# Kernel optimization log

Measured on AMD Instinct MI355X. Metric: run time of the kernel, lower is better.

Reference implementation:

```python
import jax, jax.numpy as jnp
import numpy as np

NQ = 4          # wires=4 in the PennyLane device
NLAYERS = 4     # num_layers default
AX = 'abcd'     # one einsum letter per qubit axis


def _apply_1q(state, U, w):
    """Apply a 2x2 (or batched (B,2,2)) unitary to qubit axis w of state (B,2,2,2,2)."""
    sub = AX[w]
    out = AX[:w] + 'x' + AX[w + 1:]
    if U.ndim == 3:
        return jnp.einsum(f'zx{sub},z{AX}->z{out}', U, state)
    return jnp.einsum(f'x{sub},z{AX}->z{out}', U, state)


def _apply_cnot(state, c, t):
    """CNOT with control qubit c, target qubit t (static wire indices)."""
    s0 = jax.lax.index_in_dim(state, 0, axis=c + 1, keepdims=True)
    s1 = jax.lax.index_in_dim(state, 1, axis=c + 1, keepdims=True)
    s1 = jnp.flip(s1, axis=t + 1)  # flip target amplitudes where control = 1
    return jnp.concatenate([s0, s1], axis=c + 1)


def _rot(phi, theta, omega):
    """PennyLane Rot gate: RZ(omega) @ RY(theta) @ RZ(phi), as a 2x2 complex matrix."""
    c = jnp.cos(theta * 0.5)
    s = jnp.sin(theta * 0.5)
    em = jnp.exp(-0.5j * (phi + omega))   # e^{-i(phi+omega)/2}, complex64 (weak 1j)
    ed = jnp.exp(0.5j * (phi - omega))    # e^{+i(phi-omega)/2}
    return jnp.stack([
        jnp.stack([em * c, -ed * s]),
        jnp.stack([jnp.conj(ed) * s, jnp.conj(em) * c]),
    ])


def _forward(inputs, q_weights):
    B = inputs.shape[0]
    # |0000> statevector, batched
    state = jnp.zeros((B, 2 ** NQ), jnp.complex64).at[:, 0].set(1.0)
    state = state.reshape((B,) + (2,) * NQ)

    # AngleEmbedding with rotation='Y': RY(x_w) on each wire w (per-sample angles)
    half = inputs * 0.5
    c, s = jnp.cos(half), jnp.sin(half)
    for w in range(NQ):
        U = jnp.stack([jnp.stack([c[:, w], -s[:, w]], axis=-1),
                       jnp.stack([s[:, w], c[:, w]], axis=-1)], axis=-2)
        state = _apply_1q(state, U.astype(jnp.complex64), w)

    # One StronglyEntanglingLayers block per layer of q_weights:
    # per-qubit Rot gates followed by a ring of CNOTs (range r=1 for single-layer calls)
    n_layers = q_weights.shape[0]
    for l in range(n_layers):
        for w in range(NQ):
            state = _apply_1q(state, _rot(q_weights[l, w, 0],
                                          q_weights[l, w, 1],
                                          q_weights[l, w, 2]), w)
        for w in range(NQ):
            state = _apply_cnot(state, w, (w + 1) % NQ)

    # <Z_i> for each wire: marginal prob of bit i, contracted with diag(+1,-1)
    probs = state.real ** 2 + state.imag ** 2  # (B,2,2,2,2)
    z = jnp.array([1.0, -1.0], jnp.float32)
    expvals = []
    for w in range(NQ):
        reduce_axes = tuple(i + 1 for i in range(NQ) if i != w)
        p = probs.sum(axis=reduce_axes)  # (B,2)
        expvals.append(p @ z)
    return jnp.stack(expvals, axis=-1)  # (B,4)


def setup_inputs() -> dict:
    key = jax.random.key(0)
    k1, k2 = jax.random.split(key)
    B = 1048576
    inputs = jax.random.normal(k1, (B, NQ), dtype=jnp.float32)
    # glorot_uniform for shape (4,4,3): limit = sqrt(6/(fan_in+fan_out))
    limit = np.sqrt(6.0 / (NQ * 3 + NQ * 3)).astype(np.float32)
    q_weights = jax.random.uniform(k2, (NLAYERS, NQ, 3), dtype=jnp.float32,
                                   minval=-limit, maxval=limit)
    return {"inputs": inputs, "q_weights": q_weights}


def reference(inputs, q_weights):
    return _forward(inputs, q_weights)
```

## Files before the change

kernel.cpp:

```cpp
#include <hip/hip_runtime.h>
#include <math.h>


__global__ void build_unitary(const float* __restrict__ qw, float* __restrict__ U) {
    __shared__ float g[16][8];
    int t = threadIdx.x;
    if (t < 16) {
        float phi = qw[t * 3 + 0], theta = qw[t * 3 + 1], omega = qw[t * 3 + 2];
        float ct = cosf(0.5f * theta), st = sinf(0.5f * theta);
        float ha = 0.5f * (phi + omega), hd = 0.5f * (phi - omega);
        float emr = cosf(ha), emi = -sinf(ha);
        float edr = cosf(hd), edi =  sinf(hd);
        g[t][0] =  emr * ct; g[t][1] =  emi * ct;
        g[t][2] = -edr * st; g[t][3] = -edi * st;
        g[t][4] =  edr * st; g[t][5] = -edi * st;
        g[t][6] =  emr * ct; g[t][7] = -emi * ct;
    }
    __syncthreads();
    if (t >= 16) return;
    float ar[16], ai[16];
#pragma unroll
    for (int b = 0; b < 16; ++b) { ar[b] = (b == t) ? 1.f : 0.f; ai[b] = 0.f; }
#pragma unroll
    for (int l = 0; l < 4; ++l) {
#pragma unroll
        for (int w = 0; w < 4; ++w) {
            int gi = l * 4 + w;
            float u00r = g[gi][0], u00i = g[gi][1], u01r = g[gi][2], u01i = g[gi][3];
            float u10r = g[gi][4], u10i = g[gi][5], u11r = g[gi][6], u11i = g[gi][7];
            int mask = 8 >> w;
#pragma unroll
            for (int b = 0; b < 16; ++b) {
                if (b & mask) continue;
                int b1 = b | mask;
                float xr = ar[b], xi = ai[b], yr = ar[b1], yi = ai[b1];
                ar[b]  = u00r * xr - u00i * xi + u01r * yr - u01i * yi;
                ai[b]  = u00r * xi + u00i * xr + u01r * yi + u01i * yr;
                ar[b1] = u10r * xr - u10i * xi + u11r * yr - u11i * yi;
                ai[b1] = u10r * xi + u10i * xr + u11r * yi + u11i * yr;
            }
        }
#pragma unroll
        for (int w = 0; w < 4; ++w) {
            int cm = 8 >> w, tm = 8 >> ((w + 1) & 3);
#pragma unroll
            for (int b = 0; b < 16; ++b) {
                if ((b & cm) && !(b & tm)) {
                    int b1 = b | tm;
                    float tr = ar[b], ti = ai[b];
                    ar[b] = ar[b1]; ai[b] = ai[b1];
                    ar[b1] = tr;    ai[b1] = ti;
                }
            }
        }
    }
#pragma unroll
    for (int b = 0; b < 16; ++b) {
        U[t * 32 + b]      = ar[b];
        U[t * 32 + 16 + b] = ai[b];
    }
}

__global__ __launch_bounds__(256) void qlayer_main(
        const float4* __restrict__ x, const float* __restrict__ U,
        float4* __restrict__ out, int B) {
    __shared__ float svs[256 * 17];
    int tid = threadIdx.x;
    int i = blockIdx.x * 256 + tid;
    if (i >= B) return;

    float4 xv = x[i];
    float c0, s0, c1, s1, c2, s2, c3, s3;
    __sincosf(0.5f * xv.x, &s0, &c0);
    __sincosf(0.5f * xv.y, &s1, &c1);
    __sincosf(0.5f * xv.z, &s2, &c2);
    __sincosf(0.5f * xv.w, &s3, &c3);
    float p01[4] = {c0 * c1, c0 * s1, s0 * c1, s0 * s1};
    float p23[4] = {c2 * c3, c2 * s3, s2 * c3, s2 * s3};
    float* mysv = &svs[tid * 17];
#pragma unroll
    for (int a = 0; a < 4; ++a)
#pragma unroll
        for (int b = 0; b < 4; ++b) mysv[a * 4 + b] = p01[a] * p23[b];

    float are[16], aim[16];
#pragma unroll
    for (int b = 0; b < 16; ++b) { are[b] = 0.f; aim[b] = 0.f; }
#pragma unroll 2
    for (int j = 0; j < 16; ++j) {
        float sj = mysv[j];
        const float* row = U + j * 32;
#pragma unroll
        for (int b = 0; b < 16; ++b) {
            are[b] = fmaf(row[b],      sj, are[b]);
            aim[b] = fmaf(row[16 + b], sj, aim[b]);
        }
    }

    float p[16];
#pragma unroll
    for (int b = 0; b < 16; ++b) p[b] = fmaf(are[b], are[b], aim[b] * aim[b]);

    float s8[8], d8[8];
#pragma unroll
    for (int k = 0; k < 8; ++k) { s8[k] = p[2*k] + p[2*k+1]; d8[k] = p[2*k] - p[2*k+1]; }
    float e3 = ((d8[0]+d8[1])+(d8[2]+d8[3]))+((d8[4]+d8[5])+(d8[6]+d8[7]));
    float u4[4], v4[4];
#pragma unroll
    for (int m = 0; m < 4; ++m) { u4[m] = s8[2*m] + s8[2*m+1]; v4[m] = s8[2*m] - s8[2*m+1]; }
    float e2 = (v4[0]+v4[1])+(v4[2]+v4[3]);
    float x0 = u4[0]+u4[1], x1 = u4[2]+u4[3];
    float y0 = u4[0]-u4[1], y1 = u4[2]-u4[3];
    float e1 = y0 + y1;
    float e0 = x0 - x1;

    out[i] = make_float4(e0, e1, e2, e3);
}

extern "C" void kernel_launch(void* const* d_in, const int* in_sizes, int n_in,
                              void* d_out, int out_size, void* d_ws, size_t ws_size,
                              hipStream_t stream) {
    const float4* x  = (const float4*)d_in[0];
    const float*  qw = (const float*)d_in[1];
    float* U = (float*)d_ws;
    float4* out = (float4*)d_out;
    int B = in_sizes[0] / 4;

    hipLaunchKernelGGL(build_unitary, dim3(1), dim3(64), 0, stream, qw, U);

    int blocks = (B + 255) / 256;
    hipLaunchKernelGGL(qlayer_main, dim3(blocks), dim3(256), 0, stream,
                       x, U, out, B);
}
```

Measured before the change: 92.75 us.

## Precompute Pauli-basis coefficient tensor so each sample evaluates a trigonometric polynomial

```diff
diff --git a/kernel.cpp b/kernel.cpp
--- a/kernel.cpp
+++ b/kernel.cpp
@@ -2,9 +2,13 @@
 #include <math.h>
 
 
-__global__ void build_unitary(const float* __restrict__ qw, float* __restrict__ U) {
+__global__ void build_C(const float* __restrict__ qw, float* __restrict__ Cg) {
     __shared__ float g[16][8];
+    __shared__ float Ur[16][16];
+    __shared__ float Ui[16][16];
+    __shared__ float ReE[4][16][16];
     int t = threadIdx.x;
+
     if (t < 16) {
         float phi = qw[t * 3 + 0], theta = qw[t * 3 + 1], omega = qw[t * 3 + 2];
         float ct = cosf(0.5f * theta), st = sinf(0.5f * theta);
@@ -17,103 +21,126 @@
         g[t][6] =  emr * ct; g[t][7] = -emi * ct;
     }
     __syncthreads();
-    if (t >= 16) return;
-    float ar[16], ai[16];
+
+    if (t < 16) {
+        float ar[16], ai[16];
 #pragma unroll
-    for (int b = 0; b < 16; ++b) { ar[b] = (b == t) ? 1.f : 0.f; ai[b] = 0.f; }
+        for (int b = 0; b < 16; ++b) { ar[b] = (b == t) ? 1.f : 0.f; ai[b] = 0.f; }
 #pragma unroll
-    for (int l = 0; l < 4; ++l) {
+        for (int l = 0; l < 4; ++l) {
 #pragma unroll
-        for (int w = 0; w < 4; ++w) {
-            int gi = l * 4 + w;
-            float u00r = g[gi][0], u00i = g[gi][1], u01r = g[gi][2], u01i = g[gi][3];
-            float u10r = g[gi][4], u10i = g[gi][5], u11r = g[gi][6], u11i = g[gi][7];
-            int mask = 8 >> w;
+            for (int w = 0; w < 4; ++w) {
+                int gi = l * 4 + w;
+                float u00r = g[gi][0], u00i = g[gi][1], u01r = g[gi][2], u01i = g[gi][3];
+                float u10r = g[gi][4], u10i = g[gi][5], u11r = g[gi][6], u11i = g[gi][7];
+                int mask = 8 >> w;
 #pragma unroll
-            for (int b = 0; b < 16; ++b) {
-                if (b & mask) continue;
-                int b1 = b | mask;
-                float xr = ar[b], xi = ai[b], yr = ar[b1], yi = ai[b1];
-                ar[b]  = u00r * xr - u00i * xi + u01r * yr - u01i * yi;
-                ai[b]  = u00r * xi + u00i * xr + u01r * yi + u01i * yr;
-                ar[b1] = u10r * xr - u10i * xi + u11r * yr - u11i * yi;
-                ai[b1] = u10r * xi + u10i * xr + u11r * yi + u11i * yr;
+                for (int b = 0; b < 16; ++b) {
+                    if (b & mask) continue;
+                    int b1 = b | mask;
+                    float xr = ar[b], xi = ai[b], yr = ar[b1], yi = ai[b1];
+                    ar[b]  = u00r * xr - u00i * xi + u01r * yr - u01i * yi;
+                    ai[b]  = u00r * xi + u00i * xr + u01r * yi + u01i * yr;
+                    ar[b1] = u10r * xr - u10i * xi + u11r * yr - u11i * yi;
+                    ai[b1] = u10r * xi + u10i * xr + u11r * yi + u11i * yr;
+                }
+            }
+#pragma unroll
+            for (int w = 0; w < 4; ++w) {
+                int cm = 8 >> w, tm = 8 >> ((w + 1) & 3);
+#pragma unroll
+                for (int b = 0; b < 16; ++b) {
+                    if ((b & cm) && !(b & tm)) {
+                        int b1 = b | tm;
+                        float tr = ar[b], ti = ai[b];
+                        ar[b] = ar[b1]; ai[b] = ai[b1];
+                        ar[b1] = tr;    ai[b1] = ti;
+                    }
+                }
             }
         }
 #pragma unroll
-        for (int w = 0; w < 4; ++w) {
-            int cm = 8 >> w, tm = 8 >> ((w + 1) & 3);
+        for (int b = 0; b < 16; ++b) { Ur[b][t] = ar[b]; Ui[b][t] = ai[b]; }
+    }
+    __syncthreads();
+
+    for (int idx = t; idx < 1024; idx += 256) {
+        int w = idx >> 8, i = (idx >> 4) & 15, j = idx & 15;
+        float acc = 0.f;
 #pragma unroll
-            for (int b = 0; b < 16; ++b) {
-                if ((b & cm) && !(b & tm)) {
-                    int b1 = b | tm;
-                    float tr = ar[b], ti = ai[b];
-                    ar[b] = ar[b1]; ai[b] = ai[b1];
-                    ar[b1] = tr;    ai[b1] = ti;
-                }
-            }
+        for (int b = 0; b < 16; ++b) {
+            float z = ((b >> (3 - w)) & 1) ? -1.f : 1.f;
+            acc += z * (Ur[b][i] * Ur[b][j] + Ui[b][i] * Ui[b][j]);
         }
+        ReE[w][i][j] = acc;
     }
+    __syncthreads();
+
+    for (int idx = t; idx < 324; idx += 256) {
+        int w = idx & 3, tt = idx >> 2;
+        int t01 = tt / 9, t23 = tt % 9;
+        int tq[4] = { t01 / 3, t01 % 3, t23 / 3, t23 % 3 };
+        int xmask = 0, zmask = 0;
 #pragma unroll
-    for (int b = 0; b < 16; ++b) {
-        U[t * 32 + b]      = ar[b];
-        U[t * 32 + 16 + b] = ai[b];
+        for (int k = 0; k < 4; ++k) {
+            if (tq[k] == 1) xmask |= 8 >> k;
+            if (tq[k] == 2) zmask |= 8 >> k;
+        }
+        float acc = 0.f;
+#pragma unroll
+        for (int i = 0; i < 16; ++i) {
+            float sgn = (__popc(i & zmask) & 1) ? -1.f : 1.f;
+            acc += sgn * ReE[w][i][i ^ xmask];
+        }
+        Cg[idx] = acc * 0.0625f;
     }
 }
 
 __global__ __launch_bounds__(256) void qlayer_main(
-        const float4* __restrict__ x, const float* __restrict__ U,
+        const float4* __restrict__ x, const float* __restrict__ Cg,
         float4* __restrict__ out, int B) {
-    __shared__ float svs[256 * 17];
-    int tid = threadIdx.x;
-    int i = blockIdx.x * 256 + tid;
+    __shared__ __align__(16) float C[324];
+    for (int k = threadIdx.x; k < 324; k += 256) C[k] = Cg[k];
+    __syncthreads();
+
+    int i = blockIdx.x * 256 + threadIdx.x;
     if (i >= B) return;
+    float4 xv = x[i];
+    float s0, c0, s1, c1, s2, c2, s3, c3;
+    __sincosf(xv.x, &s0, &c0);
+    __sincosf(xv.y, &s1, &c1);
+    __sincosf(xv.z, &s2, &c2);
+    __sincosf(xv.w, &s3, &c3);
+    float m0[3] = {1.f, s0, c0}, m1[3] = {1.f, s1, c1};
+    float m2[3] = {1.f, s2, c2}, m3[3] = {1.f, s3, c3};
+    float M01[9], M23[9];
+#pragma unroll
+    for (int a = 0; a < 3; ++a)
+#pragma unroll
+        for (int b = 0; b < 3; ++b) {
+            M01[a * 3 + b] = m0[a] * m1[b];
+            M23[a * 3 + b] = m2[a] * m3[b];
+        }
 
-    float4 xv = x[i];
-    float c0, s0, c1, s1, c2, s2, c3, s3;
-    __sincosf(0.5f * xv.x, &s0, &c0);
-    __sincosf(0.5f * xv.y, &s1, &c1);
-    __sincosf(0.5f * xv.z, &s2, &c2);
-    __sincosf(0.5f * xv.w, &s3, &c3);
-    float p01[4] = {c0 * c1, c0 * s1, s0 * c1, s0 * s1};
-    float p23[4] = {c2 * c3, c2 * s3, s2 * c3, s2 * s3};
-    float* mysv = &svs[tid * 17];
+    float e0 = 0.f, e1 = 0.f, e2 = 0.f, e3 = 0.f;
 #pragma unroll
-    for (int a = 0; a < 4; ++a)
+    for (int t01 = 0; t01 < 9; ++t01) {
+        float h0 = 0.f, h1 = 0.f, h2 = 0.f, h3 = 0.f;
 #pragma unroll
-        for (int b = 0; b < 4; ++b) mysv[a * 4 + b] = p01[a] * p23[b];
-
-    float are[16], aim[16];
-#pragma unroll
-    for (int b = 0; b < 16; ++b) { are[b] = 0.f; aim[b] = 0.f; }
-#pragma unroll 2
-    for (int j = 0; j < 16; ++j) {
-        float sj = mysv[j];
-        const float* row = U + j * 32;
-#pragma unroll
-        for (int b = 0; b < 16; ++b) {
-            are[b] = fmaf(row[b],      sj, are[b]);
-            aim[b] = fmaf(row[16 + b], sj, aim[b]);
+        for (int t23 = 0; t23 < 9; ++t23) {
+            const float4 c4 = *(const float4*)&C[(t01 * 9 + t23) * 4];
+            float mv = M23[t23];
+            h0 = fmaf(c4.x, mv, h0);
+            h1 = fmaf(c4.y, mv, h1);
+            h2 = fmaf(c4.z, mv, h2);
+            h3 = fmaf(c4.w, mv, h3);
         }
+        float mu = M01[t01];
+        e0 = fmaf(mu, h0, e0);
+        e1 = fmaf(mu, h1, e1);
+        e2 = fmaf(mu, h2, e2);
+        e3 = fmaf(mu, h3, e3);
     }
-
-    float p[16];
-#pragma unroll
-    for (int b = 0; b < 16; ++b) p[b] = fmaf(are[b], are[b], aim[b] * aim[b]);
-
-    float s8[8], d8[8];
-#pragma unroll
-    for (int k = 0; k < 8; ++k) { s8[k] = p[2*k] + p[2*k+1]; d8[k] = p[2*k] - p[2*k+1]; }
-    float e3 = ((d8[0]+d8[1])+(d8[2]+d8[3]))+((d8[4]+d8[5])+(d8[6]+d8[7]));
-    float u4[4], v4[4];
-#pragma unroll
-    for (int m = 0; m < 4; ++m) { u4[m] = s8[2*m] + s8[2*m+1]; v4[m] = s8[2*m] - s8[2*m+1]; }
-    float e2 = (v4[0]+v4[1])+(v4[2]+v4[3]);
-    float x0 = u4[0]+u4[1], x1 = u4[2]+u4[3];
-    float y0 = u4[0]-u4[1], y1 = u4[2]-u4[3];
-    float e1 = y0 + y1;
-    float e0 = x0 - x1;
-
     out[i] = make_float4(e0, e1, e2, e3);
 }
 
@@ -122,13 +149,13 @@
                               hipStream_t stream) {
     const float4* x  = (const float4*)d_in[0];
     const float*  qw = (const float*)d_in[1];
-    float* U = (float*)d_ws;
+    float* Cg = (float*)d_ws;
     float4* out = (float4*)d_out;
     int B = in_sizes[0] / 4;
 
-    hipLaunchKernelGGL(build_unitary, dim3(1), dim3(64), 0, stream, qw, U);
+    hipLaunchKernelGGL(build_C, dim3(1), dim3(256), 0, stream, qw, Cg);
 
     int blocks = (B + 255) / 256;
     hipLaunchKernelGGL(qlayer_main, dim3(blocks), dim3(256), 0, stream,
-                       x, U, out, B);
+                       x, Cg, out, B);
 }
```

Result: faster. 84.55 us (-8.8%).
